# Performance work log

Hardware: AMD Instinct MI355X
Metric: run time of the kernel (lower is better)

Reference implementation:

```python
import jax, jax.numpy as jnp
import numpy as np

B, T, H, D = 2, 2048, 32, 128
Q_GROUP = 4
H_KV = H // Q_GROUP
INNER = H * D
KV_INNER = H_KV * D
ATTN_SCALE = 1.0 / np.sqrt(D)
NEG = -30000.0


def setup_inputs() -> dict:
    key = jax.random.key(0)
    ks = jax.random.split(key, 6)
    stm = jax.random.normal(ks[0], (B, T, H, D), dtype=jnp.float32)
    wq = jax.random.normal(ks[1], (INNER, INNER), dtype=jnp.float32) * 0.02
    wk = jax.random.normal(ks[2], (INNER, KV_INNER), dtype=jnp.float32) * 0.02
    wv = jax.random.normal(ks[3], (INNER, KV_INNER), dtype=jnp.float32) * 0.02
    wo = jax.random.normal(ks[4], (INNER, INNER), dtype=jnp.float32) * 0.02
    # RoPE tables (Mistral convention: emb = cat(freqs, freqs))
    inv_freq = 1.0 / (10000.0 ** (jnp.arange(0, D, 2, dtype=jnp.float32) / D))
    freqs = jnp.arange(T, dtype=jnp.float32)[:, None] * inv_freq[None, :]  # [T, D/2]
    emb = jnp.concatenate([freqs, freqs], axis=-1)  # [T, D]
    cos = jnp.cos(emb)
    sin = jnp.sin(emb)
    # affine causal mask: attn*mask_w + mask_b
    tril = jnp.tril(jnp.ones((T, T), dtype=jnp.float32))
    mask_w = tril
    mask_b = (1.0 - tril) * NEG
    return {"stm": stm, "wq": wq, "wk": wk, "wv": wv, "wo": wo,
            "cos": cos, "sin": sin, "mask_w": mask_w, "mask_b": mask_b}


def _rope(x, cos, sin):
    # x: [B, T, H, D]; rotate-half: split last dim, cat(-right, left)
    half = x.shape[-1] // 2
    l, r = x[..., :half], x[..., half:]
    x2 = jnp.concatenate([-r, l], axis=-1)
    return x * cos[None, :, None, :] + x2 * sin[None, :, None, :]


def reference(stm, wq, wk, wv, wo, cos, sin, mask_w, mask_b):
    x = stm.reshape(B * T, INNER)
    q = (x @ wq).reshape(B, T, H, D)
    k = (x @ wk).reshape(B, T, H_KV, D)
    v = (x @ wv).reshape(B, T, H_KV, D)
    # GQA: repeat_interleave KV heads by q_group -> [B, T, H, D]
    k = jnp.repeat(k, Q_GROUP, axis=2)
    v = jnp.repeat(v, Q_GROUP, axis=2)
    q = _rope(q, cos, sin)
    k = _rope(k, cos, sin)
    # QK^T in fp32, affine causal mask, softmax
    attn = jnp.einsum('bqhd,bkhd->bhqk', q, k).astype(jnp.float32) * ATTN_SCALE
    attn = attn * mask_w[None, None] + mask_b[None, None]
    attn = jax.nn.softmax(attn, axis=3).astype(stm.dtype)
    o = jnp.einsum('bhqk,bkhd->bqhd', attn, v)
    out = (o.reshape(B * T, INNER) @ wo).reshape(B, T, H, D)
    return out
```

## Files before the change

kernel.cpp:

```cpp
#include <hip/hip_runtime.h>
#include <hip/hip_bf16.h>

typedef unsigned short u16;
typedef unsigned int   u32;
using bf16x8 = __attribute__((ext_vector_type(8))) short;
using f32x4  = __attribute__((ext_vector_type(4))) float;

#define T_N    2048
#define NQKV   6144
#define ATTN_SCALE 0.08838834764831845f

__device__ __forceinline__ u16 f2bf(float f) {
  union { float f; u32 u; } v; v.f = f;
  u32 r = v.u + 0x7fffu + ((v.u >> 16) & 1u);
  return (u16)(r >> 16);
}

__device__ __forceinline__ void gl_lds16(const void* g, void* l) {
  __builtin_amdgcn_global_load_lds(
      (const __attribute__((address_space(1))) u32*)g,
      (__attribute__((address_space(3))) u32*)l, 16, 0, 0);
}

__global__ void cvt_f32_bf16(const float* __restrict__ in, u16* __restrict__ out, int n8) {
  int i = blockIdx.x * blockDim.x + threadIdx.x;
  if (i >= n8) return;
  const float4* p = (const float4*)in + (size_t)i * 2;
  float4 a = p[0], b = p[1];
  union { u16 s[8]; uint4 v; } u;
  u.s[0] = f2bf(a.x); u.s[1] = f2bf(a.y); u.s[2] = f2bf(a.z); u.s[3] = f2bf(a.w);
  u.s[4] = f2bf(b.x); u.s[5] = f2bf(b.y); u.s[6] = f2bf(b.z); u.s[7] = f2bf(b.w);
  ((uint4*)out)[i] = u.v;
}

__global__ void transpose_cvt(const float* __restrict__ in, u16* __restrict__ out,
                              int R, int C) {
  __shared__ float tile[32][33];
  const int r0 = blockIdx.x * 32, c0 = blockIdx.y * 32;
  const int tx = threadIdx.x, ty = threadIdx.y;
#pragma unroll
  for (int i = 0; i < 4; ++i)
    tile[ty + 8 * i][tx] = in[(size_t)(r0 + ty + 8 * i) * C + c0 + tx];
  __syncthreads();
#pragma unroll
  for (int i = 0; i < 4; ++i)
    out[(size_t)(c0 + ty + 8 * i) * R + r0 + tx] = f2bf(tile[tx][ty + 8 * i]);
}

__global__ void gemm_bf16(const u16* __restrict__ A, const u16* __restrict__ BT,
                          float* __restrict__ C, int N, int K) {
  __shared__ __align__(16) u16 lds[2][16][64][8];
  const int tid  = threadIdx.x;
  const int w    = tid >> 6, lane = tid & 63;
  const int r    = lane & 15, kg = lane >> 4;
  const int bm   = blockIdx.y * 128, bn = blockIdx.x * 128;
  const int wr   = w >> 1, wc = w & 1;

  const u16* srcs[4];
#pragma unroll
  for (int i = 0; i < 4; ++i) {
    const int s = w * 4 + i;
    if (s < 8) srcs[i] = A  + (size_t)(bm + s * 16 + r) * K + kg * 8;
    else       srcs[i] = BT + (size_t)(bn + (s - 8) * 16 + r) * K + kg * 8;
  }

  f32x4 acc[4][4];
#pragma unroll
  for (int i = 0; i < 4; ++i)
#pragma unroll
    for (int j = 0; j < 4; ++j) acc[i][j] = (f32x4){0.f, 0.f, 0.f, 0.f};

  const int nk = K >> 5;
#pragma unroll
  for (int i = 0; i < 4; ++i)
    gl_lds16(srcs[i], &lds[0][w * 4 + i][0][0]);
  __syncthreads();

  for (int kt = 0; kt < nk; ++kt) {
    const int bi = kt & 1;
    if (kt + 1 < nk) {
      const int koff = (kt + 1) * 32;
#pragma unroll
      for (int i = 0; i < 4; ++i)
        gl_lds16(srcs[i] + koff, &lds[bi ^ 1][w * 4 + i][0][0]);
    }
    bf16x8 af[4], bfg[4];
#pragma unroll
    for (int i = 0; i < 4; ++i)
      af[i] = *(const bf16x8*)&lds[bi][wr * 4 + i][lane][0];
#pragma unroll
    for (int j = 0; j < 4; ++j)
      bfg[j] = *(const bf16x8*)&lds[bi][8 + wc * 4 + j][lane][0];
#pragma unroll
    for (int i = 0; i < 4; ++i)
#pragma unroll
      for (int j = 0; j < 4; ++j)
        acc[i][j] = __builtin_amdgcn_mfma_f32_16x16x32_bf16(af[i], bfg[j], acc[i][j], 0, 0, 0);
    __syncthreads();
  }

#pragma unroll
  for (int i = 0; i < 4; ++i) {
    const int row0 = bm + wr * 64 + i * 16 + kg * 4;
#pragma unroll
    for (int j = 0; j < 4; ++j) {
      const int col = bn + wc * 64 + j * 16 + r;
#pragma unroll
      for (int e = 0; e < 4; ++e)
        C[(size_t)(row0 + e) * N + col] = acc[i][j][e];
    }
  }
}

__global__ void rope_pack(const float* __restrict__ QKV,
                          const float* __restrict__ cosb, const float* __restrict__ sinb,
                          u16* __restrict__ Qb, u16* __restrict__ Kb) {
  const int bt = blockIdx.x;
  const int b = bt >> 11, t = bt & 2047;
  const float* row = QKV + (size_t)bt * NQKV;
  const int d    = threadIdx.x & 127;
  const int half = threadIdx.x >> 7;
  const float c = cosb[t * 128 + d];
  const float s = sinb[t * 128 + d];
#pragma unroll
  for (int pass = 0; pass < 20; ++pass) {
    const int hh = pass * 2 + half;
    const int col = (hh < 32) ? hh * 128 + d : 4096 + (hh - 32) * 128 + d;
    const float x  = row[col];
    const float xp = (d < 64) ? -row[col + 64] : row[col - 64];
    const float v  = x * c + xp * s;
    if (hh < 32)
      Qb[((size_t)(b * 32 + hh) * 2048 + t) * 128 + d] = f2bf(v * ATTN_SCALE);
    else
      Kb[((size_t)(b * 8 + (hh - 32)) * 2048 + t) * 128 + d] = f2bf(v);
  }
}

__global__ void v_transpose(const float* __restrict__ QKV, u16* __restrict__ Vt) {
  __shared__ float tile[32][33];
  const int bkh = blockIdx.z;
  const int b = bkh >> 3, kh = bkh & 7;
  const int t0 = blockIdx.x * 32, d0 = blockIdx.y * 32;
  const int tx = threadIdx.x, ty = threadIdx.y;
#pragma unroll
  for (int i = 0; i < 4; ++i) {
    const int t = t0 + ty + 8 * i;
    tile[ty + 8 * i][tx] = QKV[(size_t)(b * 2048 + t) * NQKV + 5120 + kh * 128 + d0 + tx];
  }
  __syncthreads();
#pragma unroll
  for (int i = 0; i < 4; ++i) {
    const int d = d0 + ty + 8 * i;
    Vt[((size_t)bkh * 128 + d) * 2048 + t0 + tx] = f2bf(tile[tx][ty + 8 * i]);
  }
}

__global__ __launch_bounds__(512) void attn_fwd(
    const u16* __restrict__ Qb, const u16* __restrict__ Kb,
    const u16* __restrict__ Vt, u16* __restrict__ Ob) {
  const int pair = blockIdx.x;
  const int bh   = blockIdx.y;
  const int b = bh >> 5, h = bh & 31;
  const int bkh = b * 8 + (h >> 2);
  const int tid = threadIdx.x;
  const int w = tid >> 6, lane = tid & 63;
  const int r = lane & 15, kg = lane >> 4;

  const u16*  Qp0 = Qb + (size_t)bh * 2048 * 128;
  const char* Kp  = (const char*)(Kb + (size_t)bkh * 2048 * 128);
  const char* Vp  = (const char*)(Vt + (size_t)bkh * 128 * 2048);

  __shared__ __align__(16) char k_lds[2][64 * 256];
  __shared__ __align__(16) char v_lds[128 * 128];
  __shared__ __align__(16) u16  p_lds[8][16][72];
  u16 (*pl)[72] = p_lds[w];

  const int swz = (r & 7) << 4;

#pragma unroll 1
  for (int ph = 0; ph < 2; ++ph) {
    const int qt = ph ? 15 - pair : pair;
    const int q0 = qt * 128 + w * 16;
    const int nk = (qt + 1) * 2;

    bf16x8 qf[4];
    {
      const u16* Qp = Qp0 + (size_t)q0 * 128;
#pragma unroll
      for (int ks = 0; ks < 4; ++ks)
        qf[ks] = *(const bf16x8*)(Qp + r * 128 + ks * 32 + kg * 8);
    }

    f32x4 oacc[8];
#pragma unroll
    for (int dt = 0; dt < 8; ++dt) oacc[dt] = (f32x4){0.f, 0.f, 0.f, 0.f};
    float m_run[4] = {-1e30f, -1e30f, -1e30f, -1e30f};
    float l_run[4] = {0.f, 0.f, 0.f, 0.f};

#pragma unroll
    for (int i = 0; i < 2; ++i) {
      const int o = tid * 16 + i * 8192;
      const int row = o >> 8, colb = o & 255;
      gl_lds16(Kp + (size_t)row * 256 + (colb ^ ((row & 7) << 4)), k_lds[0] + o);
    }
    __syncthreads();
    int cur = 0;

    for (int kt = 0; kt < nk; ++kt) {
      const int k0 = kt * 64;
#pragma unroll
      for (int i = 0; i < 2; ++i) {
        const int o = tid * 16 + i * 8192;
        const int row = o >> 7, colb = o & 127;
        gl_lds16(Vp + (size_t)row * 4096 + (size_t)k0 * 2 + (colb ^ ((row & 7) << 4)),
                 v_lds + o);
      }
      if (kt + 1 < nk) {
        const int k0n = (kt + 1) * 64;
#pragma unroll
        for (int i = 0; i < 2; ++i) {
          const int o = tid * 16 + i * 8192;
          const int row = o >> 8, colb = o & 255;
          gl_lds16(Kp + (size_t)(k0n + row) * 256 + (colb ^ ((row & 7) << 4)),
                   k_lds[cur ^ 1] + o);
        }
      }

      f32x4 s[4];
#pragma unroll
      for (int nt = 0; nt < 4; ++nt) s[nt] = (f32x4){0.f, 0.f, 0.f, 0.f};
#pragma unroll
      for (int nt = 0; nt < 4; ++nt) {
        const char* kb = k_lds[cur] + (nt * 16 + r) * 256;
#pragma unroll
        for (int ks = 0; ks < 4; ++ks) {
          bf16x8 kf = *(const bf16x8*)(kb + ((ks * 64 + kg * 16) ^ swz));
          s[nt] = __builtin_amdgcn_mfma_f32_16x16x32_bf16(qf[ks], kf, s[nt], 0, 0, 0);
        }
      }

      if (k0 + 63 > q0) {
#pragma unroll
        for (int nt = 0; nt < 4; ++nt) {
          const int kcol = k0 + nt * 16 + r;
#pragma unroll
          for (int e = 0; e < 4; ++e)
            if (kcol > q0 + kg * 4 + e) s[nt][e] = -1e30f;
        }
      }

      float sf[4];
#pragma unroll
      for (int e = 0; e < 4; ++e) {
        float v = fmaxf(fmaxf(s[0][e], s[1][e]), fmaxf(s[2][e], s[3][e]));
        v = fmaxf(v, __shfl_xor(v, 1));
        v = fmaxf(v, __shfl_xor(v, 2));
        v = fmaxf(v, __shfl_xor(v, 4));
        v = fmaxf(v, __shfl_xor(v, 8));
        const float mn = fmaxf(m_run[e], v);
        sf[e] = __expf(m_run[e] - mn);
        m_run[e] = mn;
      }
      float rs[4] = {0.f, 0.f, 0.f, 0.f};
#pragma unroll
      for (int nt = 0; nt < 4; ++nt)
#pragma unroll
        for (int e = 0; e < 4; ++e) {
          const float p = __expf(s[nt][e] - m_run[e]);
          s[nt][e] = p;
          rs[e] += p;
        }
#pragma unroll
      for (int e = 0; e < 4; ++e) {
        float v = rs[e];
        v += __shfl_xor(v, 1); v += __shfl_xor(v, 2);
        v += __shfl_xor(v, 4); v += __shfl_xor(v, 8);
        l_run[e] = l_run[e] * sf[e] + v;
      }
#pragma unroll
      for (int dt = 0; dt < 8; ++dt)
#pragma unroll
        for (int e = 0; e < 4; ++e) oacc[dt][e] *= sf[e];

      __syncthreads();

#pragma unroll
      for (int nt = 0; nt < 4; ++nt)
#pragma unroll
        for (int e = 0; e < 4; ++e)
          pl[kg * 4 + e][nt * 16 + r] = f2bf(s[nt][e]);
      asm volatile("" ::: "memory");
#pragma unroll
      for (int kstep = 0; kstep < 2; ++kstep) {
        bf16x8 pf = *(const bf16x8*)&pl[r][kstep * 32 + kg * 8];
#pragma unroll
        for (int dt = 0; dt < 8; ++dt) {
          const char* vb = v_lds + (dt * 16 + r) * 128 + ((kstep * 64 + kg * 16) ^ swz);
          bf16x8 vf = *(const bf16x8*)vb;
          oacc[dt] = __builtin_amdgcn_mfma_f32_16x16x32_bf16(pf, vf, oacc[dt], 0, 0, 0);
        }
      }
      asm volatile("" ::: "memory");
      __syncthreads();
      cur ^= 1;
    }

    float inv[4];
#pragma unroll
    for (int e = 0; e < 4; ++e) inv[e] = 1.0f / l_run[e];
    const size_t orow0 = (size_t)(b * 2048 + q0 + kg * 4);
#pragma unroll
    for (int dt = 0; dt < 8; ++dt)
#pragma unroll
      for (int e = 0; e < 4; ++e)
        Ob[(orow0 + e) * 4096 + h * 128 + dt * 16 + r] = f2bf(oacc[dt][e] * inv[e]);
    __syncthreads();
  }
}

extern "C" void kernel_launch(void* const* d_in, const int* in_sizes, int n_in,
                              void* d_out, int out_size, void* d_ws, size_t ws_size,
                              hipStream_t stream) {
  const float* stm  = (const float*)d_in[0];
  const float* wq   = (const float*)d_in[1];
  const float* wk   = (const float*)d_in[2];
  const float* wv   = (const float*)d_in[3];
  const float* wo   = (const float*)d_in[4];
  const float* cosb = (const float*)d_in[5];
  const float* sinb = (const float*)d_in[6];
  float* out = (float*)d_out;

  char* ws = (char*)d_ws;
  u16*   Xb    = (u16*)(ws + 0);
  u16*   WcatT = (u16*)(ws + 33554432);
  u16*   WoT   = (u16*)(ws + 83886080);
  float* QKV   = (float*)(ws + 117440512);
  u16*   Qb    = (u16*)(ws + 218103808);
  u16*   Kb    = (u16*)(ws + 251658240);
  u16*   Vt    = (u16*)(ws + 260046848);

  cvt_f32_bf16<<<8192, 256, 0, stream>>>(stm, Xb, 2097152);
  transpose_cvt<<<dim3(128, 128), dim3(32, 8), 0, stream>>>(wq, WcatT, 4096, 4096);
  transpose_cvt<<<dim3(128, 32),  dim3(32, 8), 0, stream>>>(wk, WcatT + (size_t)4096 * 4096, 4096, 1024);
  transpose_cvt<<<dim3(128, 32),  dim3(32, 8), 0, stream>>>(wv, WcatT + (size_t)5120 * 4096, 4096, 1024);
  transpose_cvt<<<dim3(128, 128), dim3(32, 8), 0, stream>>>(wo, WoT, 4096, 4096);

  gemm_bf16<<<dim3(48, 32), 256, 0, stream>>>(Xb, WcatT, QKV, NQKV, 4096);

  rope_pack<<<4096, 256, 0, stream>>>(QKV, cosb, sinb, Qb, Kb);
  v_transpose<<<dim3(64, 4, 16), dim3(32, 8), 0, stream>>>(QKV, Vt);

  attn_fwd<<<dim3(8, 64), 512, 0, stream>>>(Qb, Kb, Vt, Xb );

  gemm_bf16<<<dim3(32, 32), 256, 0, stream>>>(Xb, WoT, out, 4096, 4096);
}
```

Baseline: 1.069 ms.

## Replace GEMM with 256x256 tiled kernel using swizzled LDS and XCD remap

Replaces the 128x128 tile, BK=32 bf16 GEMM with a 256x256 tile, BK=64 kernel using 512 threads, 8 waves and 128 KB of double-buffered LDS. It adds an XOR swizzle on LDS layout to avoid bank conflicts, a block-id remap so neighbouring tiles land on the same XCD for L2 reuse, and s_setprio around the MFMA bursts. The aim is higher arithmetic intensity and fewer global loads per MFMA in both projection GEMMs. The trade-offs are heavy register and LDS pressure, which limit occupancy, and tail effects from the smaller grid of 384 and 256 blocks.

```diff
diff --git a/kernel.cpp b/kernel.cpp
--- a/kernel.cpp
+++ b/kernel.cpp
@@ -47,69 +47,97 @@
     out[(size_t)(c0 + ty + 8 * i) * R + r0 + tx] = f2bf(tile[tx][ty + 8 * i]);
 }
 
-__global__ void gemm_bf16(const u16* __restrict__ A, const u16* __restrict__ BT,
-                          float* __restrict__ C, int N, int K) {
-  __shared__ __align__(16) u16 lds[2][16][64][8];
-  const int tid  = threadIdx.x;
-  const int w    = tid >> 6, lane = tid & 63;
-  const int r    = lane & 15, kg = lane >> 4;
-  const int bm   = blockIdx.y * 128, bn = blockIdx.x * 128;
-  const int wr   = w >> 1, wc = w & 1;
-
-  const u16* srcs[4];
-#pragma unroll
-  for (int i = 0; i < 4; ++i) {
-    const int s = w * 4 + i;
-    if (s < 8) srcs[i] = A  + (size_t)(bm + s * 16 + r) * K + kg * 8;
-    else       srcs[i] = BT + (size_t)(bn + (s - 8) * 16 + r) * K + kg * 8;
-  }
-
-  f32x4 acc[4][4];
-#pragma unroll
-  for (int i = 0; i < 4; ++i)
+__global__ __launch_bounds__(512, 2) void gemm256_bf16(
+    const u16* __restrict__ A, const u16* __restrict__ BT,
+    float* __restrict__ C, int N, int K, int nbx) {
+  __shared__ __align__(16) char lA[2][32768];
+  __shared__ __align__(16) char lB[2][32768];
+  const int tid = threadIdx.x;
+  const int w = tid >> 6, lane = tid & 63;
+  const int r = lane & 15, kg = lane >> 4;
+  const int wm = w >> 2, wn = w & 3;
+
+  int bid = blockIdx.x;
+  const int cpx = gridDim.x >> 3;
+  bid = (bid & 7) * cpx + (bid >> 3);
+  const int bx = bid % nbx, by = bid / nbx;
+
+  const size_t Kb = (size_t)K * 2;
+  const char* Ab = (const char*)A  + (size_t)(by << 8) * Kb;
+  const char* Bb = (const char*)BT + (size_t)(bx << 8) * Kb;
+
+  const int o1 = tid * 16, o2 = o1 + 8192;
+  const int sr1 = o1 >> 7, sc1 = (o1 & 127) ^ ((sr1 & 7) << 4);
+  const int sr2 = o2 >> 7, sc2 = (o2 & 127) ^ ((sr2 & 7) << 4);
+
+#define STAGE256(buf, ktb)                                                       \
+  do {                                                                           \
+    gl_lds16(Ab + (size_t)sr1 * Kb + (ktb) + sc1, &lA[buf][o1]);                 \
+    gl_lds16(Ab + (size_t)sr2 * Kb + (ktb) + sc2, &lA[buf][o2]);                 \
+    gl_lds16(Ab + (size_t)(128 + sr1) * Kb + (ktb) + sc1, &lA[buf][16384 + o1]); \
+    gl_lds16(Ab + (size_t)(128 + sr2) * Kb + (ktb) + sc2, &lA[buf][16384 + o2]); \
+    gl_lds16(Bb + (size_t)sr1 * Kb + (ktb) + sc1, &lB[buf][o1]);                 \
+    gl_lds16(Bb + (size_t)sr2 * Kb + (ktb) + sc2, &lB[buf][o2]);                 \
+    gl_lds16(Bb + (size_t)(128 + sr1) * Kb + (ktb) + sc1, &lB[buf][16384 + o1]); \
+    gl_lds16(Bb + (size_t)(128 + sr2) * Kb + (ktb) + sc2, &lB[buf][16384 + o2]); \
+  } while (0)
+
+  f32x4 acc[8][4];
+#pragma unroll
+  for (int i = 0; i < 8; ++i)
 #pragma unroll
     for (int j = 0; j < 4; ++j) acc[i][j] = (f32x4){0.f, 0.f, 0.f, 0.f};
 
-  const int nk = K >> 5;
-#pragma unroll
-  for (int i = 0; i < 4; ++i)
-    gl_lds16(srcs[i], &lds[0][w * 4 + i][0][0]);
+  const int nk = K >> 6;
+  STAGE256(0, 0);
   __syncthreads();
 
+  const int swz = (r & 7) << 4;
+#pragma unroll 2
   for (int kt = 0; kt < nk; ++kt) {
-    const int bi = kt & 1;
-    if (kt + 1 < nk) {
-      const int koff = (kt + 1) * 32;
-#pragma unroll
-      for (int i = 0; i < 4; ++i)
-        gl_lds16(srcs[i] + koff, &lds[bi ^ 1][w * 4 + i][0][0]);
-    }
-    bf16x8 af[4], bfg[4];
-#pragma unroll
-    for (int i = 0; i < 4; ++i)
-      af[i] = *(const bf16x8*)&lds[bi][wr * 4 + i][lane][0];
-#pragma unroll
-    for (int j = 0; j < 4; ++j)
-      bfg[j] = *(const bf16x8*)&lds[bi][8 + wc * 4 + j][lane][0];
-#pragma unroll
-    for (int i = 0; i < 4; ++i)
-#pragma unroll
-      for (int j = 0; j < 4; ++j)
-        acc[i][j] = __builtin_amdgcn_mfma_f32_16x16x32_bf16(af[i], bfg[j], acc[i][j], 0, 0, 0);
+    const int cur = kt & 1;
+    if (kt + 1 < nk) STAGE256(cur ^ 1, (size_t)(kt + 1) << 7);
+    const char* pa = lA[cur] + wm * 16384 + r * 128;
+    const char* pb = lB[cur] + wn * 8192 + r * 128;
+    bf16x8 bfr[4][2];
+#pragma unroll
+    for (int ni = 0; ni < 4; ++ni)
+#pragma unroll
+      for (int ks = 0; ks < 2; ++ks)
+        bfr[ni][ks] = *(const bf16x8*)(pb + ni * 2048 + ((ks * 64 + kg * 16) ^ swz));
+#pragma unroll
+    for (int p = 0; p < 4; ++p) {
+      bf16x8 af[2][2];
+#pragma unroll
+      for (int m2 = 0; m2 < 2; ++m2)
+#pragma unroll
+        for (int ks = 0; ks < 2; ++ks)
+          af[m2][ks] = *(const bf16x8*)(pa + (p * 2 + m2) * 2048 + ((ks * 64 + kg * 16) ^ swz));
+      __builtin_amdgcn_s_setprio(1);
+#pragma unroll
+      for (int m2 = 0; m2 < 2; ++m2)
+#pragma unroll
+        for (int ni = 0; ni < 4; ++ni)
+#pragma unroll
+          for (int ks = 0; ks < 2; ++ks)
+            acc[p * 2 + m2][ni] = __builtin_amdgcn_mfma_f32_16x16x32_bf16(
+                af[m2][ks], bfr[ni][ks], acc[p * 2 + m2][ni], 0, 0, 0);
+      __builtin_amdgcn_s_setprio(0);
+    }
     __syncthreads();
   }
-
-#pragma unroll
-  for (int i = 0; i < 4; ++i) {
-    const int row0 = bm + wr * 64 + i * 16 + kg * 4;
-#pragma unroll
-    for (int j = 0; j < 4; ++j) {
-      const int col = bn + wc * 64 + j * 16 + r;
-#pragma unroll
-      for (int e = 0; e < 4; ++e)
-        C[(size_t)(row0 + e) * N + col] = acc[i][j][e];
-    }
-  }
+#undef STAGE256
+
+  float* Cp = C + (size_t)((by << 8) + wm * 128 + kg * 4) * N + (bx << 8) + wn * 64 + r;
+#pragma unroll
+  for (int mi = 0; mi < 8; ++mi)
+#pragma unroll
+    for (int e = 0; e < 4; ++e) {
+      float* rowp = Cp + (size_t)(mi * 16 + e) * N;
+#pragma unroll
+      for (int ni = 0; ni < 4; ++ni)
+        rowp[ni * 16] = acc[mi][ni][e];
+    }
 }
 
 __global__ void rope_pack(const float* __restrict__ QKV,
@@ -345,12 +373,12 @@
   transpose_cvt<<<dim3(128, 32),  dim3(32, 8), 0, stream>>>(wv, WcatT + (size_t)5120 * 4096, 4096, 1024);
   transpose_cvt<<<dim3(128, 128), dim3(32, 8), 0, stream>>>(wo, WoT, 4096, 4096);
 
-  gemm_bf16<<<dim3(48, 32), 256, 0, stream>>>(Xb, WcatT, QKV, NQKV, 4096);
+  gemm256_bf16<<<384, 512, 0, stream>>>(Xb, WcatT, QKV, NQKV, 4096, 24);
 
   rope_pack<<<4096, 256, 0, stream>>>(QKV, cosb, sinb, Qb, Kb);
   v_transpose<<<dim3(64, 4, 16), dim3(32, 8), 0, stream>>>(QKV, Vt);
 
   attn_fwd<<<dim3(8, 64), 512, 0, stream>>>(Qb, Kb, Vt, Xb );
 
-  gemm_bf16<<<dim3(32, 32), 256, 0, stream>>>(Xb, WoT, out, 4096, 4096);
-}
+  gemm256_bf16<<<256, 512, 0, stream>>>(Xb, WoT, out, 4096, 4096, 16);
+}
```

Result: faster. 872.4 us (-18.4%).
